# Performance work log

Measured on AMD Instinct MI355X. Metric: run time of the kernel, lower is better.

## Reference

```python
import jax, jax.numpy as jnp
import numpy as np
from jax import lax

EPS = 1e-5
NUM_BITS = 8          # activation quantization bits
NUM_BITS_WEIGHT = 8   # weight quantization bits


def fake_quant(x, bits):
    """Uniform min-max quantize-dequantize (per-tensor), STE on round."""
    mn = jnp.min(x)
    mx = jnp.max(x)
    scale = jnp.maximum((mx - mn) / (2 ** bits - 1), jnp.asarray(1e-8, x.dtype))
    q = jnp.round((x - mn) / scale) * scale + mn
    # straight-through estimator: identity gradient through rounding
    return x + lax.stop_gradient(q - x)


def batchnorm(x, gamma, beta, mean, var):
    # x: [N, C, H, W]; stats per channel C (eval mode, running stats)
    inv = gamma / jnp.sqrt(var + EPS)
    return x * inv[None, :, None, None] + (beta - mean * inv)[None, :, None, None]


def qconv(x, w, padding):
    xq = fake_quant(x, NUM_BITS)
    wq = fake_quant(w, NUM_BITS_WEIGHT)
    return lax.conv_general_dilated(
        xq, wq, window_strides=(1, 1), padding=padding,
        dimension_numbers=("NCHW", "OIHW", "NCHW"))


def setup_inputs() -> dict:
    key = jax.random.key(0)
    ks = jax.random.split(key, 8)
    C_in, bn_size, growth = 512, 4, 32
    C_mid = bn_size * growth  # 128
    N, H, W = 64, 28, 28
    x = jax.random.normal(ks[0], (N, C_in, H, W), dtype=jnp.float32)
    gamma1 = jax.random.uniform(ks[1], (C_in,), minval=0.5, maxval=1.5)
    beta1 = jax.random.normal(ks[2], (C_in,)) * 0.1
    mean1 = jax.random.normal(ks[3], (C_in,)) * 0.1
    var1 = jax.random.uniform(ks[4], (C_in,), minval=0.5, maxval=1.5)
    w1 = jax.random.normal(ks[5], (C_mid, C_in, 1, 1)) * (1.0 / np.sqrt(C_in))
    gamma2 = jax.random.uniform(ks[6], (C_mid,), minval=0.5, maxval=1.5)
    beta2 = jax.random.normal(ks[7], (C_mid,)) * 0.1
    mean2 = jax.random.normal(jax.random.fold_in(key, 10), (C_mid,)) * 0.1
    var2 = jax.random.uniform(jax.random.fold_in(key, 11), (C_mid,), minval=0.5, maxval=1.5)
    w2 = jax.random.normal(jax.random.fold_in(key, 12), (growth, C_mid, 3, 3)) * (1.0 / np.sqrt(C_mid * 9))
    return {"x": x, "gamma1": gamma1, "beta1": beta1, "mean1": mean1, "var1": var1,
            "w1": w1, "gamma2": gamma2, "beta2": beta2, "mean2": mean2, "var2": var2,
            "w2": w2}


def reference(x, gamma1, beta1, mean1, var1, w1, gamma2, beta2, mean2, var2, w2):
    h = jax.nn.relu(batchnorm(x, gamma1, beta1, mean1, var1))
    h = qconv(h, w1, padding=((0, 0), (0, 0)))            # 1x1 conv, 512 -> 128
    h = jax.nn.relu(batchnorm(h, gamma2, beta2, mean2, var2))
    h = qconv(h, w2, padding=((1, 1), (1, 1)))            # 3x3 conv, 128 -> 32
    # drop_rate == 0 -> dropout is identity
    return h
```

## Files before the change

### kernel.cpp

```cpp
#include <hip/hip_runtime.h>

typedef unsigned short u16;
typedef unsigned short u16x4 __attribute__((ext_vector_type(4)));
typedef unsigned short u16x8 __attribute__((ext_vector_type(8)));
typedef short bf16x8 __attribute__((ext_vector_type(8)));
typedef float f32x4 __attribute__((ext_vector_type(4)));

#define EPSF 1e-5f

#define NB   64
#define C1   512
#define C2   128
#define C3   32
#define HH   28
#define WW   28
#define HW   784
#define NHW  50176
#define XELEMS 25690112
#define K1_BLOCKS 2048
#define CONV1_BLOCKS 392
#define CONV2_BLOCKS 784

#define WS_BN1I   64
#define WS_BN1B   2112
#define WS_BN2I   4160
#define WS_BN2B   4672
#define WS_WQ1    5376
#define WS_WQ2    136448
#define WS_P1     210176
#define WS_P2     226560
#define WS_PW1    232832
#define WS_PW2    233344
#define WS_H2     233472

__device__ __forceinline__ float bf2f(u16 u) { return __uint_as_float(((unsigned)u) << 16); }
__device__ __forceinline__ u16 f2bf(float f) {
  unsigned x = __float_as_uint(f);
  return (u16)((x + 0x7fffu + ((x >> 16) & 1u)) >> 16);
}
__device__ __forceinline__ float finz(float f) {
  unsigned u = __float_as_uint(f);
  return ((u & 0x7f800000u) == 0x7f800000u) ? 0.0f : f;
}

__device__ __forceinline__ void block_minmax(float& mn, float& mx) {
  for (int m = 32; m; m >>= 1) {
    mn = fminf(mn, __shfl_xor(mn, m));
    mx = fmaxf(mx, __shfl_xor(mx, m));
  }
  __shared__ float wmn[4], wmx[4];
  const int wv = threadIdx.x >> 6;
  if ((threadIdx.x & 63) == 0) { wmn[wv] = mn; wmx[wv] = mx; }
  __syncthreads();
  if (threadIdx.x == 0) {
    mn = fminf(fminf(wmn[0], wmn[1]), fminf(wmn[2], wmn[3]));
    mx = fmaxf(fmaxf(wmx[0], wmx[1]), fmaxf(wmx[2], wmx[3]));
  }
}

__global__ __launch_bounds__(256) void kwA_kernel(const float* g1, const float* be1,
                                                  const float* m1, const float* v1,
                                                  const float* w1,
                                                  const float* g2, const float* be2,
                                                  const float* m2, const float* v2,
                                                  const float* w2, unsigned char* ws) {
  const int t = threadIdx.x;
  const int b = blockIdx.x;
  float2* pw1 = (float2*)(ws + WS_PW1);
  float2* pw2 = (float2*)(ws + WS_PW2);

  if (b == 80) {
    float* bn1i = (float*)(ws + WS_BN1I);
    float* bn1b = (float*)(ws + WS_BN1B);
    float* bn2i = (float*)(ws + WS_BN2I);
    float* bn2b = (float*)(ws + WS_BN2B);
    for (int c = t; c < C1; c += 256) {
      float inv = g1[c] / sqrtf(v1[c] + EPSF);
      bn1i[c] = inv;
      bn1b[c] = be1[c] - m1[c] * inv;
    }
    if (t < C2) {
      float inv = g2[t] / sqrtf(v2[t] + EPSF);
      bn2i[t] = inv;
      bn2b[t] = be2[t] - m2[t] * inv;
    }
    return;
  }

  float mn = 3.4e38f, mx = -3.4e38f;
  if (b < 64) {
    f32x4 v = *(const f32x4*)(w1 + b * 1024 + t * 4);
#pragma unroll
    for (int j = 0; j < 4; j++) {
      float f = finz(v[j]); mn = fminf(mn, f); mx = fmaxf(mx, f);
    }
    block_minmax(mn, mx);
    if (t == 0) pw1[b] = make_float2(mn, mx);
  } else {
    const int base = (b - 64) * 2304;
#pragma unroll
    for (int j = 0; j < 9; j++) {
      float f = finz(w2[base + t + j * 256]); mn = fminf(mn, f); mx = fmaxf(mx, f);
    }
    block_minmax(mn, mx);
    if (t == 0) pw2[b - 64] = make_float2(mn, mx);
  }
}

__global__ __launch_bounds__(256) void kwB_kernel(const float* w1, const float* w2,
                                                  unsigned char* ws) {
  const float2* pw1 = (const float2*)(ws + WS_PW1);
  const float2* pw2 = (const float2*)(ws + WS_PW2);
  u16* wq1 = (u16*)(ws + WS_WQ1);
  u16* wq2 = (u16*)(ws + WS_WQ2);
  const int t = threadIdx.x;
  const int b = blockIdx.x;
  __shared__ float bc[2];

  if (b < 64) {
    if (t < 64) {
      float2 p = pw1[t];
      float mn = p.x, mx = p.y;
      for (int m = 32; m; m >>= 1) {
        mn = fminf(mn, __shfl_xor(mn, m));
        mx = fmaxf(mx, __shfl_xor(mx, m));
      }
      if (t == 0) { bc[0] = mn; bc[1] = mx; }
    }
    __syncthreads();
    const float mn = bc[0];
    const float s = fmaxf((bc[1] - mn) / 255.0f, 1e-8f);
    const float rs = 1.0f / s;
    f32x4 v = *(const f32x4*)(w1 + b * 1024 + t * 4);
    u16x4 o;
#pragma unroll
    for (int j = 0; j < 4; j++)
      o[j] = f2bf(fmaf(rintf((finz(v[j]) - mn) * rs), s, mn));
    *(u16x4*)(wq1 + b * 1024 + t * 4) = o;
  } else {
    if (t < 64) {
      float2 p = (t < 16) ? pw2[t] : make_float2(3.4e38f, -3.4e38f);
      float mn = p.x, mx = p.y;
      for (int m = 32; m; m >>= 1) {
        mn = fminf(mn, __shfl_xor(mn, m));
        mx = fmaxf(mx, __shfl_xor(mx, m));
      }
      if (t == 0) { bc[0] = mn; bc[1] = mx; }
    }
    __syncthreads();
    const float mn = bc[0];
    const float s = fmaxf((bc[1] - mn) / 255.0f, 1e-8f);
    const float rs = 1.0f / s;
    const int base = (b - 64) * 2304;
#pragma unroll
    for (int j = 0; j < 9; j++) {
      int o = base + t + j * 256;
      int tap = o >> 12;
      int rem = o & 4095;
      float f = finz(w2[rem * 9 + tap]);
      wq2[o] = f2bf(fmaf(rintf((f - mn) * rs), s, mn));
    }
  }
}

__global__ __launch_bounds__(256) void k1_minmax(const float* __restrict__ x, unsigned char* ws) {
  const float* bn1i = (const float*)(ws + WS_BN1I);
  const float* bn1b = (const float*)(ws + WS_BN1B);
  float2* p1 = (float2*)(ws + WS_P1);
  int gid = blockIdx.x * blockDim.x + threadIdx.x;
  int stride = gridDim.x * blockDim.x;
  const int ngroups = XELEMS / 4;
  float mn = 3.4e38f, mx = 0.0f;
  for (int i = gid; i < ngroups; i += stride) {
    int base = i * 4;
    int c = (base / HW) & (C1 - 1);
    float inv = bn1i[c], bb = bn1b[c];
    f32x4 u = *((const f32x4*)x + i);
#pragma unroll
    for (int j = 0; j < 4; j++) {
      float f = fmaxf(fmaf(u[j], inv, bb), 0.0f);
      mn = fminf(mn, f); mx = fmaxf(mx, f);
    }
  }
  block_minmax(mn, mx);
  if (threadIdx.x == 0) p1[blockIdx.x] = make_float2(mn, mx);
}

__global__ __launch_bounds__(256) void conv1_kernel(const float* __restrict__ x,
                                                    unsigned char* ws) {
  const float* bn1i = (const float*)(ws + WS_BN1I);
  const float* bn1b = (const float*)(ws + WS_BN1B);
  const float* bn2i = (const float*)(ws + WS_BN2I);
  const float* bn2b = (const float*)(ws + WS_BN2B);
  const u16* wq1 = (const u16*)(ws + WS_WQ1);
  const float2* p1 = (const float2*)(ws + WS_P1);
  float2* p2 = (float2*)(ws + WS_P2);
  u16* h2 = (u16*)(ws + WS_H2);

  __shared__ __align__(16) u16 Alds[2][128 * 40];
  __shared__ __align__(16) u16 Blds[2][128 * 40];
  __shared__ float bc[2];
  __shared__ float wred[8];

  const int t = threadIdx.x;
  const int sp0 = blockIdx.x * 128;

  {
    float* rmn = (float*)&Alds[0][0];
    float* rmx = (float*)&Blds[0][0];
    const f32x4* p4 = (const f32x4*)p1;
    float mn = 3.4e38f, mx = 0.0f;
#pragma unroll
    for (int i = 0; i < 4; i++) {
      f32x4 v = p4[t + i * 256];
      mn = fminf(mn, fminf(v[0], v[2]));
      mx = fmaxf(mx, fmaxf(v[1], v[3]));
    }
    rmn[t] = mn; rmx[t] = mx;
    __syncthreads();
    for (int s = 128; s > 0; s >>= 1) {
      if (t < s) { rmn[t] = fminf(rmn[t], rmn[t + s]); rmx[t] = fmaxf(rmx[t], rmx[t + s]); }
      __syncthreads();
    }
    if (t == 0) { bc[0] = rmn[0]; bc[1] = rmx[0]; }
    __syncthreads();
  }
  const float mn1 = bc[0];
  const float s1 = fmaxf((bc[1] - mn1) / 255.0f, 1e-8f);
  const float r1 = 1.0f / s1;

  const int kk = t >> 3;
  const int spA = (t & 7) * 8;
  const int spB = 64 + spA;
  const int ga = sp0 + spA, gb = sp0 + spB;
  const int na = ga / HW, hwa = ga % HW;
  const int nb = gb / HW, hwb = gb % HW;
  const float* xA = x + na * (C1 * HW) + hwa;
  const float* xB = x + nb * (C1 * HW) + hwb;
  const int colg = (kk & 7) + 8 * ((((kk >> 3) + (spA >> 3))) & 3);

  const int wco = t >> 1;
  const int wko = (t & 1) * 16;
  const int ab0 = wko >> 3;
  const int aswz = (wco >> 3) & 3;

  const int lane = t & 63;
  const int l15 = lane & 15;
  const int q = lane >> 4;
  const int wv = t >> 6;
  const int wy = wv >> 1;
  const int wx = wv & 1;

  f32x4 acc[4][4] = {};

  u16x8 a0 = *(const u16x8*)(wq1 + wco * C1 + wko);
  u16x8 a1 = *(const u16x8*)(wq1 + wco * C1 + wko + 8);
  f32x4 va0 = *(const f32x4*)(xA + kk * HW);
  f32x4 va1 = *(const f32x4*)(xA + kk * HW + 4);
  f32x4 vb0 = *(const f32x4*)(xB + kk * HW);
  f32x4 vb1 = *(const f32x4*)(xB + kk * HW + 4);
  float inv = bn1i[kk], bb = bn1b[kk];

#pragma unroll 1
  for (int i = 0; i < 16; i++) {
    const int cur = i & 1;
    *(u16x8*)&Alds[cur][wco * 40 + (((ab0 + 0 + aswz) & 3) << 3)] = a0;
    *(u16x8*)&Alds[cur][wco * 40 + (((ab0 + 1 + aswz) & 3) << 3)] = a1;
#pragma unroll
    for (int j = 0; j < 4; j++) {
      float f0 = fmaxf(fmaf(va0[j], inv, bb), 0.0f);
      Blds[cur][(spA + j) * 40 + colg] = f2bf(fmaf(rintf((f0 - mn1) * r1), s1, mn1));
      float f1 = fmaxf(fmaf(va1[j], inv, bb), 0.0f);
      Blds[cur][(spA + 4 + j) * 40 + colg] = f2bf(fmaf(rintf((f1 - mn1) * r1), s1, mn1));
      float g0 = fmaxf(fmaf(vb0[j], inv, bb), 0.0f);
      Blds[cur][(spB + j) * 40 + colg] = f2bf(fmaf(rintf((g0 - mn1) * r1), s1, mn1));
      float g1v = fmaxf(fmaf(vb1[j], inv, bb), 0.0f);
      Blds[cur][(spB + 4 + j) * 40 + colg] = f2bf(fmaf(rintf((g1v - mn1) * r1), s1, mn1));
    }
    if (i < 15) {
      const int kn = (i + 1) * 32;
      a0 = *(const u16x8*)(wq1 + wco * C1 + kn + wko);
      a1 = *(const u16x8*)(wq1 + wco * C1 + kn + wko + 8);
      const int c = kn + kk;
      va0 = *(const f32x4*)(xA + c * HW);
      va1 = *(const f32x4*)(xA + c * HW + 4);
      vb0 = *(const f32x4*)(xB + c * HW);
      vb1 = *(const f32x4*)(xB + c * HW + 4);
      inv = bn1i[c]; bb = bn1b[c];
    }
    __syncthreads();
    bf16x8 af[4], bfr[4];
#pragma unroll
    for (int ii = 0; ii < 4; ii++) {
      int R = wy * 64 + ii * 16 + l15;
      af[ii] = *(const bf16x8*)&Alds[cur][R * 40 + (((q + (R >> 3)) & 3) << 3)];
    }
#pragma unroll
    for (int j = 0; j < 4; j++) {
      int R = wx * 64 + j * 16 + l15;
      bfr[j] = *(const bf16x8*)&Blds[cur][R * 40 + (((q + (R >> 3)) & 3) << 3)];
    }
#pragma unroll
    for (int ii = 0; ii < 4; ii++)
#pragma unroll
      for (int j = 0; j < 4; j++)
        acc[ii][j] = __builtin_amdgcn_mfma_f32_16x16x32_bf16(af[ii], bfr[j], acc[ii][j], 0, 0, 0);
  }

  float lmn = 3.4e38f, lmx = 0.0f;
#pragma unroll
  for (int i = 0; i < 4; i++) {
    int cob = wy * 64 + i * 16 + q * 4;
    f32x4 i2 = *(const f32x4*)&bn2i[cob];
    f32x4 b2 = *(const f32x4*)&bn2b[cob];
#pragma unroll
    for (int j = 0; j < 4; j++) {
      int sp = sp0 + wx * 64 + j * 16 + l15;
      u16x4 v;
#pragma unroll
      for (int r = 0; r < 4; r++) {
        float h = fmaxf(fmaf(acc[i][j][r], i2[r], b2[r]), 0.0f);
        v[r] = f2bf(h);
        lmn = fminf(lmn, h); lmx = fmaxf(lmx, h);
      }
      *(u16x4*)&h2[sp * C2 + cob] = v;
    }
  }
  for (int m = 32; m; m >>= 1) {
    lmn = fminf(lmn, __shfl_xor(lmn, m));
    lmx = fmaxf(lmx, __shfl_xor(lmx, m));
  }
  if (lane == 0) { wred[wv] = lmn; wred[4 + wv] = lmx; }
  __syncthreads();
  if (t == 0) {
    float2 pr;
    pr.x = fminf(fminf(wred[0], wred[1]), fminf(wred[2], wred[3]));
    pr.y = fmaxf(fmaxf(wred[4], wred[5]), fmaxf(wred[6], wred[7]));
    p2[blockIdx.x] = pr;
  }
}

__global__ __launch_bounds__(256) void conv2_kernel(const unsigned char* ws,
                                                    float* __restrict__ out) {
  const u16* wq2 = (const u16*)(ws + WS_WQ2);
  const u16* h2 = (const u16*)(ws + WS_H2);
  const float2* p2 = (const float2*)(ws + WS_P2);
  __shared__ float bc2[2];

  const int t = threadIdx.x;
  {
    float mn = 3.4e38f, mx = 0.0f;
    for (int i = t; i < CONV1_BLOCKS; i += 256) {
      float2 p = p2[i];
      mn = fminf(mn, p.x); mx = fmaxf(mx, p.y);
    }
    block_minmax(mn, mx);
    if (t == 0) { bc2[0] = mn; bc2[1] = mx; }
    __syncthreads();
  }
  const float mn2 = bc2[0];
  const float s2 = fmaxf((bc2[1] - mn2) / 255.0f, 1e-8f);
  const float r2 = 1.0f / s2;

  const int lane = t & 63;
  const int l15 = lane & 15;
  const int q = lane >> 4;
  const int wv = t >> 6;

  const int B = blockIdx.x;
  const int sblk = (B & 7) * 98 + (B >> 3);
  const int spf = sblk * 64 + wv * 16 + l15;
  const int nn = spf / HW;
  const int hwf = spf % HW;
  const int hf = hwf / WW;
  const int wf = hwf % WW;

  f32x4 acc[2] = {};
  bf16x8 bz;
#pragma unroll
  for (int j = 0; j < 8; j++) bz[j] = 0;

  for (int tap = 0; tap < 9; tap++) {
    const int dh = tap / 3 - 1, dw = tap % 3 - 1;
    const u16* wA = wq2 + tap * (C3 * C2);
    unsigned h2i = (unsigned)(hf + dh);
    unsigned w2i = (unsigned)(wf + dw);
    const bool val = (h2i < 28u) && (w2i < 28u);
    const u16* bptr = h2 + ((size_t)(nn * HW + (int)h2i * WW + (int)w2i)) * C2;
#pragma unroll
    for (int ks = 0; ks < C2; ks += 32) {
      bf16x8 a[2], b;
#pragma unroll
      for (int f = 0; f < 2; f++)
        a[f] = *(const bf16x8*)(wA + (f * 16 + l15) * C2 + ks + q * 8);
      if (val) {
        u16x8 hv = *(const u16x8*)(bptr + ks + q * 8);
#pragma unroll
        for (int j = 0; j < 8; j++) {
          float h = bf2f(hv[j]);
          b[j] = (short)f2bf(fmaf(rintf((h - mn2) * r2), s2, mn2));
        }
      } else {
        b = bz;
      }
#pragma unroll
      for (int i = 0; i < 2; i++)
        acc[i] = __builtin_amdgcn_mfma_f32_16x16x32_bf16(a[i], b, acc[i], 0, 0, 0);
    }
  }

#pragma unroll
  for (int i = 0; i < 2; i++) {
    int co = i * 16 + q * 4;
#pragma unroll
    for (int r = 0; r < 4; r++)
      out[(nn * C3 + co + r) * HW + hwf] = acc[i][r];
  }
}

extern "C" void kernel_launch(void* const* d_in, const int* in_sizes, int n_in,
                              void* d_out, int out_size, void* d_ws, size_t ws_size,
                              hipStream_t stream) {
  const float* x  = (const float*)d_in[0];
  const float* g1 = (const float*)d_in[1];
  const float* b1 = (const float*)d_in[2];
  const float* m1 = (const float*)d_in[3];
  const float* v1 = (const float*)d_in[4];
  const float* w1 = (const float*)d_in[5];
  const float* g2 = (const float*)d_in[6];
  const float* b2 = (const float*)d_in[7];
  const float* m2 = (const float*)d_in[8];
  const float* v2 = (const float*)d_in[9];
  const float* w2 = (const float*)d_in[10];
  unsigned char* ws = (unsigned char*)d_ws;
  float* out = (float*)d_out;

  kwA_kernel<<<81, 256, 0, stream>>>(g1, b1, m1, v1, w1, g2, b2, m2, v2, w2, ws);
  kwB_kernel<<<80, 256, 0, stream>>>(w1, w2, ws);
  k1_minmax<<<K1_BLOCKS, 256, 0, stream>>>(x, ws);
  conv1_kernel<<<CONV1_BLOCKS, 256, 0, stream>>>(x, ws);
  conv2_kernel<<<CONV2_BLOCKS, 256, 0, stream>>>(ws, out);
}
```

Measured before the change: 249.2 us.

## Fuse all stages into one persistent kernel with grid barriers

Measured after the change: 591.0 us. 2.37x slower.

```diff
diff --git a/kernel.cpp b/kernel.cpp
--- a/kernel.cpp
+++ b/kernel.cpp
@@ -8,7 +8,6 @@
 
 #define EPSF 1e-5f
 
-#define NB   64
 #define C1   512
 #define C2   128
 #define C3   32
@@ -17,20 +16,20 @@
 #define HW   784
 #define NHW  50176
 #define XELEMS 25690112
-#define K1_BLOCKS 2048
+#define NGROUPS 6422528
+
+#define GRID 512
+#define XBLOCKS 510
+#define W1_BLOCK 510
+#define W2_BLOCK 511
 #define CONV1_BLOCKS 392
-#define CONV2_BLOCKS 784
-
-#define WS_BN1I   64
-#define WS_BN1B   2112
-#define WS_BN2I   4160
-#define WS_BN2B   4672
+#define CONV2_JOBS 784
+
 #define WS_WQ1    5376
 #define WS_WQ2    136448
 #define WS_P1     210176
 #define WS_P2     226560
-#define WS_PW1    232832
-#define WS_PW2    233344
+#define WS_BAR    229696
 #define WS_H2     233472
 
 __device__ __forceinline__ float bf2f(u16 u) { return __uint_as_float(((unsigned)u) << 16); }
@@ -58,363 +57,344 @@
   }
 }
 
-__global__ __launch_bounds__(256) void kwA_kernel(const float* g1, const float* be1,
-                                                  const float* m1, const float* v1,
-                                                  const float* w1,
-                                                  const float* g2, const float* be2,
-                                                  const float* m2, const float* v2,
-                                                  const float* w2, unsigned char* ws) {
+__device__ __forceinline__ void grid_barrier(unsigned* bar, unsigned target) {
+  __syncthreads();
+  if (threadIdx.x == 0) {
+    __threadfence();
+    __hip_atomic_fetch_add(bar, 1u, __ATOMIC_ACQ_REL, __HIP_MEMORY_SCOPE_AGENT);
+    while (__hip_atomic_load(bar, __ATOMIC_ACQUIRE, __HIP_MEMORY_SCOPE_AGENT) < target) {
+      __builtin_amdgcn_s_sleep(2);
+    }
+  }
+  __syncthreads();
+  __threadfence();
+}
+
+__global__ void bar_init_kernel(unsigned char* ws) {
+  if (threadIdx.x == 0) {
+    __hip_atomic_store((unsigned*)(ws + WS_BAR), 0u, __ATOMIC_RELEASE,
+                       __HIP_MEMORY_SCOPE_AGENT);
+  }
+}
+
+__global__ __launch_bounds__(256, 2) void fused_kernel(
+    const float* __restrict__ x, const float* g1, const float* be1,
+    const float* m1, const float* v1, const float* w1,
+    const float* g2, const float* be2, const float* m2, const float* v2,
+    const float* w2, unsigned char* ws, float* __restrict__ out) {
+  __shared__ __align__(16) u16 Alds[2][128 * 40];
+  __shared__ __align__(16) u16 Blds[2][128 * 40];
+  __shared__ float bn1iL[C1], bn1bL[C1];
+  __shared__ float bn2iL[C2], bn2bL[C2];
+  __shared__ float bc[2];
+  __shared__ float wred[8];
+
   const int t = threadIdx.x;
-  const int b = blockIdx.x;
-  float2* pw1 = (float2*)(ws + WS_PW1);
-  float2* pw2 = (float2*)(ws + WS_PW2);
-
-  if (b == 80) {
-    float* bn1i = (float*)(ws + WS_BN1I);
-    float* bn1b = (float*)(ws + WS_BN1B);
-    float* bn2i = (float*)(ws + WS_BN2I);
-    float* bn2b = (float*)(ws + WS_BN2B);
-    for (int c = t; c < C1; c += 256) {
-      float inv = g1[c] / sqrtf(v1[c] + EPSF);
-      bn1i[c] = inv;
-      bn1b[c] = be1[c] - m1[c] * inv;
-    }
-    if (t < C2) {
-      float inv = g2[t] / sqrtf(v2[t] + EPSF);
-      bn2i[t] = inv;
-      bn2b[t] = be2[t] - m2[t] * inv;
-    }
-    return;
-  }
-
-  float mn = 3.4e38f, mx = -3.4e38f;
-  if (b < 64) {
-    f32x4 v = *(const f32x4*)(w1 + b * 1024 + t * 4);
-#pragma unroll
-    for (int j = 0; j < 4; j++) {
-      float f = finz(v[j]); mn = fminf(mn, f); mx = fmaxf(mx, f);
-    }
-    block_minmax(mn, mx);
-    if (t == 0) pw1[b] = make_float2(mn, mx);
-  } else {
-    const int base = (b - 64) * 2304;
-#pragma unroll
-    for (int j = 0; j < 9; j++) {
-      float f = finz(w2[base + t + j * 256]); mn = fminf(mn, f); mx = fmaxf(mx, f);
-    }
-    block_minmax(mn, mx);
-    if (t == 0) pw2[b - 64] = make_float2(mn, mx);
-  }
-}
-
-__global__ __launch_bounds__(256) void kwB_kernel(const float* w1, const float* w2,
-                                                  unsigned char* ws) {
-  const float2* pw1 = (const float2*)(ws + WS_PW1);
-  const float2* pw2 = (const float2*)(ws + WS_PW2);
+  const int bid = blockIdx.x;
+
+  float2* p1 = (float2*)(ws + WS_P1);
+  float2* p2 = (float2*)(ws + WS_P2);
   u16* wq1 = (u16*)(ws + WS_WQ1);
   u16* wq2 = (u16*)(ws + WS_WQ2);
-  const int t = threadIdx.x;
-  const int b = blockIdx.x;
-  __shared__ float bc[2];
-
-  if (b < 64) {
-    if (t < 64) {
-      float2 p = pw1[t];
-      float mn = p.x, mx = p.y;
-      for (int m = 32; m; m >>= 1) {
-        mn = fminf(mn, __shfl_xor(mn, m));
-        mx = fmaxf(mx, __shfl_xor(mx, m));
-      }
+  u16* h2 = (u16*)(ws + WS_H2);
+  unsigned* bar = (unsigned*)(ws + WS_BAR);
+
+  for (int c = t; c < C1; c += 256) {
+    float inv = g1[c] / sqrtf(v1[c] + EPSF);
+    bn1iL[c] = inv;
+    bn1bL[c] = be1[c] - m1[c] * inv;
+  }
+  if (t < C2) {
+    float inv = g2[t] / sqrtf(v2[t] + EPSF);
+    bn2iL[t] = inv;
+    bn2bL[t] = be2[t] - m2[t] * inv;
+  }
+  __syncthreads();
+
+  if (bid < XBLOCKS) {
+    const f32x4* x4 = (const f32x4*)x;
+    float mn = 3.4e38f, mx = 0.0f;
+    auto proc = [&](f32x4 u, int c) {
+      float inv = bn1iL[c], bb = bn1bL[c];
+#pragma unroll
+      for (int j = 0; j < 4; j++) {
+        float f = fmaxf(fmaf(u[j], inv, bb), 0.0f);
+        mn = fminf(mn, f); mx = fmaxf(mx, f);
+      }
+    };
+    const int S = XBLOCKS * 256;
+    int i = bid * 256 + t;
+    for (; i + 3 * S < NGROUPS; i += 4 * S) {
+      f32x4 u0 = x4[i];
+      f32x4 u1 = x4[i + S];
+      f32x4 u2 = x4[i + 2 * S];
+      f32x4 u3 = x4[i + 3 * S];
+      int c0 = (i / 196) & (C1 - 1);
+      int c1 = ((i + S) / 196) & (C1 - 1);
+      int c2 = ((i + 2 * S) / 196) & (C1 - 1);
+      int c3 = ((i + 3 * S) / 196) & (C1 - 1);
+      proc(u0, c0); proc(u1, c1); proc(u2, c2); proc(u3, c3);
+    }
+    for (; i < NGROUPS; i += S) {
+      f32x4 u = x4[i];
+      proc(u, (i / 196) & (C1 - 1));
+    }
+    block_minmax(mn, mx);
+    if (t == 0) p1[bid] = make_float2(mn, mx);
+  } else if (bid == W1_BLOCK) {
+    const f32x4* w4 = (const f32x4*)w1;
+    float mn = 3.4e38f, mx = -3.4e38f;
+#pragma unroll 8
+    for (int k = t; k < 16384; k += 256) {
+      f32x4 v = w4[k];
+#pragma unroll
+      for (int j = 0; j < 4; j++) {
+        float f = finz(v[j]); mn = fminf(mn, f); mx = fmaxf(mx, f);
+      }
+    }
+    block_minmax(mn, mx);
+    if (t == 0) { bc[0] = mn; bc[1] = mx; }
+    __syncthreads();
+    const float mnv = bc[0];
+    const float s = fmaxf((bc[1] - mnv) / 255.0f, 1e-8f);
+    const float rs = 1.0f / s;
+#pragma unroll 4
+    for (int k = t; k < 16384; k += 256) {
+      f32x4 v = w4[k];
+      u16x4 o;
+#pragma unroll
+      for (int j = 0; j < 4; j++)
+        o[j] = f2bf(fmaf(rintf((finz(v[j]) - mnv) * rs), s, mnv));
+      *(u16x4*)(wq1 + k * 4) = o;
+    }
+  } else {
+    const f32x4* w4 = (const f32x4*)w2;
+    float mn = 3.4e38f, mx = -3.4e38f;
+#pragma unroll 4
+    for (int k = t; k < 9216; k += 256) {
+      f32x4 v = w4[k];
+#pragma unroll
+      for (int j = 0; j < 4; j++) {
+        float f = finz(v[j]); mn = fminf(mn, f); mx = fmaxf(mx, f);
+      }
+    }
+    block_minmax(mn, mx);
+    if (t == 0) { bc[0] = mn; bc[1] = mx; }
+    __syncthreads();
+    const float mnv = bc[0];
+    const float s = fmaxf((bc[1] - mnv) / 255.0f, 1e-8f);
+    const float rs = 1.0f / s;
+    for (int jj = t; jj < 36864; jj += 256) {
+      int tap = jj >> 12;
+      int rem = jj & 4095;
+      float f = finz(w2[rem * 9 + tap]);
+      wq2[jj] = f2bf(fmaf(rintf((f - mnv) * rs), s, mnv));
+    }
+  }
+
+  grid_barrier(bar, GRID);
+
+  if (bid < CONV1_BLOCKS) {
+    const int sp0 = bid * 128;
+
+    {
+      float mn = 3.4e38f, mx = 0.0f;
+      for (int i = t; i < XBLOCKS; i += 256) {
+        float2 p = p1[i];
+        mn = fminf(mn, p.x); mx = fmaxf(mx, p.y);
+      }
+      block_minmax(mn, mx);
       if (t == 0) { bc[0] = mn; bc[1] = mx; }
-    }
+      __syncthreads();
+    }
+    const float mn1 = bc[0];
+    const float s1 = fmaxf((bc[1] - mn1) / 255.0f, 1e-8f);
+    const float r1 = 1.0f / s1;
+
+    const int kk = t >> 3;
+    const int spA = (t & 7) * 8;
+    const int spB = 64 + spA;
+    const int ga = sp0 + spA, gb = sp0 + spB;
+    const int na = ga / HW, hwa = ga % HW;
+    const int nb = gb / HW, hwb = gb % HW;
+    const float* xA = x + na * (C1 * HW) + hwa;
+    const float* xB = x + nb * (C1 * HW) + hwb;
+    const int colg = (kk & 7) + 8 * ((((kk >> 3) + (spA >> 3))) & 3);
+
+    const int wco = t >> 1;
+    const int wko = (t & 1) * 16;
+    const int ab0 = wko >> 3;
+    const int aswz = (wco >> 3) & 3;
+
+    const int lane = t & 63;
+    const int l15 = lane & 15;
+    const int q = lane >> 4;
+    const int wv = t >> 6;
+    const int wy = wv >> 1;
+    const int wx = wv & 1;
+
+    f32x4 acc[4][4] = {};
+
+    u16x8 a0 = *(const u16x8*)(wq1 + wco * C1 + wko);
+    u16x8 a1 = *(const u16x8*)(wq1 + wco * C1 + wko + 8);
+    f32x4 va0 = *(const f32x4*)(xA + kk * HW);
+    f32x4 va1 = *(const f32x4*)(xA + kk * HW + 4);
+    f32x4 vb0 = *(const f32x4*)(xB + kk * HW);
+    f32x4 vb1 = *(const f32x4*)(xB + kk * HW + 4);
+    float inv = bn1iL[kk], bb = bn1bL[kk];
+
+#pragma unroll 1
+    for (int i = 0; i < 16; i++) {
+      const int cur = i & 1;
+      *(u16x8*)&Alds[cur][wco * 40 + (((ab0 + 0 + aswz) & 3) << 3)] = a0;
+      *(u16x8*)&Alds[cur][wco * 40 + (((ab0 + 1 + aswz) & 3) << 3)] = a1;
+#pragma unroll
+      for (int j = 0; j < 4; j++) {
+        float f0 = fmaxf(fmaf(va0[j], inv, bb), 0.0f);
+        Blds[cur][(spA + j) * 40 + colg] = f2bf(fmaf(rintf((f0 - mn1) * r1), s1, mn1));
+        float f1 = fmaxf(fmaf(va1[j], inv, bb), 0.0f);
+        Blds[cur][(spA + 4 + j) * 40 + colg] = f2bf(fmaf(rintf((f1 - mn1) * r1), s1, mn1));
+        float g0 = fmaxf(fmaf(vb0[j], inv, bb), 0.0f);
+        Blds[cur][(spB + j) * 40 + colg] = f2bf(fmaf(rintf((g0 - mn1) * r1), s1, mn1));
+        float g1v = fmaxf(fmaf(vb1[j], inv, bb), 0.0f);
+        Blds[cur][(spB + 4 + j) * 40 + colg] = f2bf(fmaf(rintf((g1v - mn1) * r1), s1, mn1));
+      }
+      if (i < 15) {
+        const int kn = (i + 1) * 32;
+        a0 = *(const u16x8*)(wq1 + wco * C1 + kn + wko);
+        a1 = *(const u16x8*)(wq1 + wco * C1 + kn + wko + 8);
+        const int c = kn + kk;
+        va0 = *(const f32x4*)(xA + c * HW);
+        va1 = *(const f32x4*)(xA + c * HW + 4);
+        vb0 = *(const f32x4*)(xB + c * HW);
+        vb1 = *(const f32x4*)(xB + c * HW + 4);
+        inv = bn1iL[c]; bb = bn1bL[c];
+      }
+      __syncthreads();
+      bf16x8 af[4], bfr[4];
+#pragma unroll
+      for (int ii = 0; ii < 4; ii++) {
+        int R = wy * 64 + ii * 16 + l15;
+        af[ii] = *(const bf16x8*)&Alds[cur][R * 40 + (((q + (R >> 3)) & 3) << 3)];
+      }
+#pragma unroll
+      for (int j = 0; j < 4; j++) {
+        int R = wx * 64 + j * 16 + l15;
+        bfr[j] = *(const bf16x8*)&Blds[cur][R * 40 + (((q + (R >> 3)) & 3) << 3)];
+      }
+#pragma unroll
+      for (int ii = 0; ii < 4; ii++)
+#pragma unroll
+        for (int j = 0; j < 4; j++)
+          acc[ii][j] = __builtin_amdgcn_mfma_f32_16x16x32_bf16(af[ii], bfr[j], acc[ii][j], 0, 0, 0);
+    }
+
+    float lmn = 3.4e38f, lmx = 0.0f;
+#pragma unroll
+    for (int i = 0; i < 4; i++) {
+      int cob = wy * 64 + i * 16 + q * 4;
+      f32x4 i2 = *(const f32x4*)&bn2iL[cob];
+      f32x4 b2 = *(const f32x4*)&bn2bL[cob];
+#pragma unroll
+      for (int j = 0; j < 4; j++) {
+        int sp = sp0 + wx * 64 + j * 16 + l15;
+        u16x4 v;
+#pragma unroll
+        for (int r = 0; r < 4; r++) {
+          float h = fmaxf(fmaf(acc[i][j][r], i2[r], b2[r]), 0.0f);
+          v[r] = f2bf(h);
+          lmn = fminf(lmn, h); lmx = fmaxf(lmx, h);
+        }
+        *(u16x4*)&h2[sp * C2 + cob] = v;
+      }
+    }
+    for (int m = 32; m; m >>= 1) {
+      lmn = fminf(lmn, __shfl_xor(lmn, m));
+      lmx = fmaxf(lmx, __shfl_xor(lmx, m));
+    }
+    if (lane == 0) { wred[wv] = lmn; wred[4 + wv] = lmx; }
     __syncthreads();
-    const float mn = bc[0];
-    const float s = fmaxf((bc[1] - mn) / 255.0f, 1e-8f);
-    const float rs = 1.0f / s;
-    f32x4 v = *(const f32x4*)(w1 + b * 1024 + t * 4);
-    u16x4 o;
-#pragma unroll
-    for (int j = 0; j < 4; j++)
-      o[j] = f2bf(fmaf(rintf((finz(v[j]) - mn) * rs), s, mn));
-    *(u16x4*)(wq1 + b * 1024 + t * 4) = o;
-  } else {
-    if (t < 64) {
-      float2 p = (t < 16) ? pw2[t] : make_float2(3.4e38f, -3.4e38f);
-      float mn = p.x, mx = p.y;
-      for (int m = 32; m; m >>= 1) {
-        mn = fminf(mn, __shfl_xor(mn, m));
-        mx = fmaxf(mx, __shfl_xor(mx, m));
-      }
+    if (t == 0) {
+      float2 pr;
+      pr.x = fminf(fminf(wred[0], wred[1]), fminf(wred[2], wred[3]));
+      pr.y = fmaxf(fmaxf(wred[4], wred[5]), fmaxf(wred[6], wred[7]));
+      p2[bid] = pr;
+    }
+  }
+
+  grid_barrier(bar, 2 * GRID);
+
+  {
+    {
+      float mn = 3.4e38f, mx = 0.0f;
+      for (int i = t; i < CONV1_BLOCKS; i += 256) {
+        float2 p = p2[i];
+        mn = fminf(mn, p.x); mx = fmaxf(mx, p.y);
+      }
+      block_minmax(mn, mx);
       if (t == 0) { bc[0] = mn; bc[1] = mx; }
-    }
-    __syncthreads();
-    const float mn = bc[0];
-    const float s = fmaxf((bc[1] - mn) / 255.0f, 1e-8f);
-    const float rs = 1.0f / s;
-    const int base = (b - 64) * 2304;
-#pragma unroll
-    for (int j = 0; j < 9; j++) {
-      int o = base + t + j * 256;
-      int tap = o >> 12;
-      int rem = o & 4095;
-      float f = finz(w2[rem * 9 + tap]);
-      wq2[o] = f2bf(fmaf(rintf((f - mn) * rs), s, mn));
-    }
-  }
-}
-
-__global__ __launch_bounds__(256) void k1_minmax(const float* __restrict__ x, unsigned char* ws) {
-  const float* bn1i = (const float*)(ws + WS_BN1I);
-  const float* bn1b = (const float*)(ws + WS_BN1B);
-  float2* p1 = (float2*)(ws + WS_P1);
-  int gid = blockIdx.x * blockDim.x + threadIdx.x;
-  int stride = gridDim.x * blockDim.x;
-  const int ngroups = XELEMS / 4;
-  float mn = 3.4e38f, mx = 0.0f;
-  for (int i = gid; i < ngroups; i += stride) {
-    int base = i * 4;
-    int c = (base / HW) & (C1 - 1);
-    float inv = bn1i[c], bb = bn1b[c];
-    f32x4 u = *((const f32x4*)x + i);
-#pragma unroll
-    for (int j = 0; j < 4; j++) {
-      float f = fmaxf(fmaf(u[j], inv, bb), 0.0f);
-      mn = fminf(mn, f); mx = fmaxf(mx, f);
-    }
-  }
-  block_minmax(mn, mx);
-  if (threadIdx.x == 0) p1[blockIdx.x] = make_float2(mn, mx);
-}
-
-__global__ __launch_bounds__(256) void conv1_kernel(const float* __restrict__ x,
-                                                    unsigned char* ws) {
-  const float* bn1i = (const float*)(ws + WS_BN1I);
-  const float* bn1b = (const float*)(ws + WS_BN1B);
-  const float* bn2i = (const float*)(ws + WS_BN2I);
-  const float* bn2b = (const float*)(ws + WS_BN2B);
-  const u16* wq1 = (const u16*)(ws + WS_WQ1);
-  const float2* p1 = (const float2*)(ws + WS_P1);
-  float2* p2 = (float2*)(ws + WS_P2);
-  u16* h2 = (u16*)(ws + WS_H2);
-
-  __shared__ __align__(16) u16 Alds[2][128 * 40];
-  __shared__ __align__(16) u16 Blds[2][128 * 40];
-  __shared__ float bc[2];
-  __shared__ float wred[8];
-
-  const int t = threadIdx.x;
-  const int sp0 = blockIdx.x * 128;
-
-  {
-    float* rmn = (float*)&Alds[0][0];
-    float* rmx = (float*)&Blds[0][0];
-    const f32x4* p4 = (const f32x4*)p1;
-    float mn = 3.4e38f, mx = 0.0f;
-#pragma unroll
-    for (int i = 0; i < 4; i++) {
-      f32x4 v = p4[t + i * 256];
-      mn = fminf(mn, fminf(v[0], v[2]));
-      mx = fmaxf(mx, fmaxf(v[1], v[3]));
-    }
-    rmn[t] = mn; rmx[t] = mx;
-    __syncthreads();
-    for (int s = 128; s > 0; s >>= 1) {
-      if (t < s) { rmn[t] = fminf(rmn[t], rmn[t + s]); rmx[t] = fmaxf(rmx[t], rmx[t + s]); }
       __syncthreads();
     }
-    if (t == 0) { bc[0] = rmn[0]; bc[1] = rmx[0]; }
-    __syncthreads();
-  }
-  const float mn1 = bc[0];
-  const float s1 = fmaxf((bc[1] - mn1) / 255.0f, 1e-8f);
-  const float r1 = 1.0f / s1;
-
-  const int kk = t >> 3;
-  const int spA = (t & 7) * 8;
-  const int spB = 64 + spA;
-  const int ga = sp0 + spA, gb = sp0 + spB;
-  const int na = ga / HW, hwa = ga % HW;
-  const int nb = gb / HW, hwb = gb % HW;
-  const float* xA = x + na * (C1 * HW) + hwa;
-  const float* xB = x + nb * (C1 * HW) + hwb;
-  const int colg = (kk & 7) + 8 * ((((kk >> 3) + (spA >> 3))) & 3);
-
-  const int wco = t >> 1;
-  const int wko = (t & 1) * 16;
-  const int ab0 = wko >> 3;
-  const int aswz = (wco >> 3) & 3;
-
-  const int lane = t & 63;
-  const int l15 = lane & 15;
-  const int q = lane >> 4;
-  const int wv = t >> 6;
-  const int wy = wv >> 1;
-  const int wx = wv & 1;
-
-  f32x4 acc[4][4] = {};
-
-  u16x8 a0 = *(const u16x8*)(wq1 + wco * C1 + wko);
-  u16x8 a1 = *(const u16x8*)(wq1 + wco * C1 + wko + 8);
-  f32x4 va0 = *(const f32x4*)(xA + kk * HW);
-  f32x4 va1 = *(const f32x4*)(xA + kk * HW + 4);
-  f32x4 vb0 = *(const f32x4*)(xB + kk * HW);
-  f32x4 vb1 = *(const f32x4*)(xB + kk * HW + 4);
-  float inv = bn1i[kk], bb = bn1b[kk];
-
-#pragma unroll 1
-  for (int i = 0; i < 16; i++) {
-    const int cur = i & 1;
-    *(u16x8*)&Alds[cur][wco * 40 + (((ab0 + 0 + aswz) & 3) << 3)] = a0;
-    *(u16x8*)&Alds[cur][wco * 40 + (((ab0 + 1 + aswz) & 3) << 3)] = a1;
-#pragma unroll
-    for (int j = 0; j < 4; j++) {
-      float f0 = fmaxf(fmaf(va0[j], inv, bb), 0.0f);
-      Blds[cur][(spA + j) * 40 + colg] = f2bf(fmaf(rintf((f0 - mn1) * r1), s1, mn1));
-      float f1 = fmaxf(fmaf(va1[j], inv, bb), 0.0f);
-      Blds[cur][(spA + 4 + j) * 40 + colg] = f2bf(fmaf(rintf((f1 - mn1) * r1), s1, mn1));
-      float g0 = fmaxf(fmaf(vb0[j], inv, bb), 0.0f);
-      Blds[cur][(spB + j) * 40 + colg] = f2bf(fmaf(rintf((g0 - mn1) * r1), s1, mn1));
-      float g1v = fmaxf(fmaf(vb1[j], inv, bb), 0.0f);
-      Blds[cur][(spB + 4 + j) * 40 + colg] = f2bf(fmaf(rintf((g1v - mn1) * r1), s1, mn1));
-    }
-    if (i < 15) {
-      const int kn = (i + 1) * 32;
-      a0 = *(const u16x8*)(wq1 + wco * C1 + kn + wko);
-      a1 = *(const u16x8*)(wq1 + wco * C1 + kn + wko + 8);
-      const int c = kn + kk;
-      va0 = *(const f32x4*)(xA + c * HW);
-      va1 = *(const f32x4*)(xA + c * HW + 4);
-      vb0 = *(const f32x4*)(xB + c * HW);
-      vb1 = *(const f32x4*)(xB + c * HW + 4);
-      inv = bn1i[c]; bb = bn1b[c];
-    }
-    __syncthreads();
-    bf16x8 af[4], bfr[4];
-#pragma unroll
-    for (int ii = 0; ii < 4; ii++) {
-      int R = wy * 64 + ii * 16 + l15;
-      af[ii] = *(const bf16x8*)&Alds[cur][R * 40 + (((q + (R >> 3)) & 3) << 3)];
-    }
-#pragma unroll
-    for (int j = 0; j < 4; j++) {
-      int R = wx * 64 + j * 16 + l15;
-      bfr[j] = *(const bf16x8*)&Blds[cur][R * 40 + (((q + (R >> 3)) & 3) << 3)];
-    }
-#pragma unroll
-    for (int ii = 0; ii < 4; ii++)
-#pragma unroll
-      for (int j = 0; j < 4; j++)
-        acc[ii][j] = __builtin_amdgcn_mfma_f32_16x16x32_bf16(af[ii], bfr[j], acc[ii][j], 0, 0, 0);
-  }
-
-  float lmn = 3.4e38f, lmx = 0.0f;
-#pragma unroll
-  for (int i = 0; i < 4; i++) {
-    int cob = wy * 64 + i * 16 + q * 4;
-    f32x4 i2 = *(const f32x4*)&bn2i[cob];
-    f32x4 b2 = *(const f32x4*)&bn2b[cob];
-#pragma unroll
-    for (int j = 0; j < 4; j++) {
-      int sp = sp0 + wx * 64 + j * 16 + l15;
-      u16x4 v;
-#pragma unroll
-      for (int r = 0; r < 4; r++) {
-        float h = fmaxf(fmaf(acc[i][j][r], i2[r], b2[r]), 0.0f);
-        v[r] = f2bf(h);
-        lmn = fminf(lmn, h); lmx = fmaxf(lmx, h);
-      }
-      *(u16x4*)&h2[sp * C2 + cob] = v;
-    }
-  }
-  for (int m = 32; m; m >>= 1) {
-    lmn = fminf(lmn, __shfl_xor(lmn, m));
-    lmx = fmaxf(lmx, __shfl_xor(lmx, m));
-  }
-  if (lane == 0) { wred[wv] = lmn; wred[4 + wv] = lmx; }
-  __syncthreads();
-  if (t == 0) {
-    float2 pr;
-    pr.x = fminf(fminf(wred[0], wred[1]), fminf(wred[2], wred[3]));
-    pr.y = fmaxf(fmaxf(wred[4], wred[5]), fmaxf(wred[6], wred[7]));
-    p2[blockIdx.x] = pr;
-  }
-}
-
-__global__ __launch_bounds__(256) void conv2_kernel(const unsigned char* ws,
-                                                    float* __restrict__ out) {
-  const u16* wq2 = (const u16*)(ws + WS_WQ2);
-  const u16* h2 = (const u16*)(ws + WS_H2);
-  const float2* p2 = (const float2*)(ws + WS_P2);
-  __shared__ float bc2[2];
-
-  const int t = threadIdx.x;
-  {
-    float mn = 3.4e38f, mx = 0.0f;
-    for (int i = t; i < CONV1_BLOCKS; i += 256) {
-      float2 p = p2[i];
-      mn = fminf(mn, p.x); mx = fmaxf(mx, p.y);
-    }
-    block_minmax(mn, mx);
-    if (t == 0) { bc2[0] = mn; bc2[1] = mx; }
-    __syncthreads();
-  }
-  const float mn2 = bc2[0];
-  const float s2 = fmaxf((bc2[1] - mn2) / 255.0f, 1e-8f);
-  const float r2 = 1.0f / s2;
-
-  const int lane = t & 63;
-  const int l15 = lane & 15;
-  const int q = lane >> 4;
-  const int wv = t >> 6;
-
-  const int B = blockIdx.x;
-  const int sblk = (B & 7) * 98 + (B >> 3);
-  const int spf = sblk * 64 + wv * 16 + l15;
-  const int nn = spf / HW;
-  const int hwf = spf % HW;
-  const int hf = hwf / WW;
-  const int wf = hwf % WW;
-
-  f32x4 acc[2] = {};
-  bf16x8 bz;
-#pragma unroll
-  for (int j = 0; j < 8; j++) bz[j] = 0;
-
-  for (int tap = 0; tap < 9; tap++) {
-    const int dh = tap / 3 - 1, dw = tap % 3 - 1;
-    const u16* wA = wq2 + tap * (C3 * C2);
-    unsigned h2i = (unsigned)(hf + dh);
-    unsigned w2i = (unsigned)(wf + dw);
-    const bool val = (h2i < 28u) && (w2i < 28u);
-    const u16* bptr = h2 + ((size_t)(nn * HW + (int)h2i * WW + (int)w2i)) * C2;
-#pragma unroll
-    for (int ks = 0; ks < C2; ks += 32) {
-      bf16x8 a[2], b;
-#pragma unroll
-      for (int f = 0; f < 2; f++)
-        a[f] = *(const bf16x8*)(wA + (f * 16 + l15) * C2 + ks + q * 8);
-      if (val) {
-        u16x8 hv = *(const u16x8*)(bptr + ks + q * 8);
-#pragma unroll
-        for (int j = 0; j < 8; j++) {
-          float h = bf2f(hv[j]);
-          b[j] = (short)f2bf(fmaf(rintf((h - mn2) * r2), s2, mn2));
+    const float mn2 = bc[0];
+    const float s2 = fmaxf((bc[1] - mn2) / 255.0f, 1e-8f);
+    const float r2 = 1.0f / s2;
+
+    const int lane = t & 63;
+    const int l15 = lane & 15;
+    const int q = lane >> 4;
+    const int wv = t >> 6;
+
+    bf16x8 bz;
+#pragma unroll
+    for (int j = 0; j < 8; j++) bz[j] = 0;
+
+    for (int job = bid; job < CONV2_JOBS; job += GRID) {
+      const int sblk = (job & 7) * 98 + (job >> 3);
+      const int spf = sblk * 64 + wv * 16 + l15;
+      const int nn = spf / HW;
+      const int hwf = spf % HW;
+      const int hf = hwf / WW;
+      const int wf = hwf % WW;
+
+      f32x4 acc[2] = {};
+
+      for (int tap = 0; tap < 9; tap++) {
+        const int dh = tap / 3 - 1, dw = tap % 3 - 1;
+        const u16* wA = wq2 + tap * (C3 * C2);
+        unsigned h2i = (unsigned)(hf + dh);
+        unsigned w2i = (unsigned)(wf + dw);
+        const bool val = (h2i < 28u) && (w2i < 28u);
+        const u16* bptr = h2 + ((size_t)(nn * HW + (int)h2i * WW + (int)w2i)) * C2;
+#pragma unroll
+        for (int ks = 0; ks < C2; ks += 32) {
+          bf16x8 a[2], b;
+#pragma unroll
+          for (int f = 0; f < 2; f++)
+            a[f] = *(const bf16x8*)(wA + (f * 16 + l15) * C2 + ks + q * 8);
+          if (val) {
+            u16x8 hv = *(const u16x8*)(bptr + ks + q * 8);
+#pragma unroll
+            for (int j = 0; j < 8; j++) {
+              float h = bf2f(hv[j]);
+              b[j] = (short)f2bf(fmaf(rintf((h - mn2) * r2), s2, mn2));
+            }
+          } else {
+            b = bz;
+          }
+#pragma unroll
+          for (int i = 0; i < 2; i++)
+            acc[i] = __builtin_amdgcn_mfma_f32_16x16x32_bf16(a[i], b, acc[i], 0, 0, 0);
         }
-      } else {
-        b = bz;
-      }
-#pragma unroll
-      for (int i = 0; i < 2; i++)
-        acc[i] = __builtin_amdgcn_mfma_f32_16x16x32_bf16(a[i], b, acc[i], 0, 0, 0);
-    }
-  }
-
-#pragma unroll
-  for (int i = 0; i < 2; i++) {
-    int co = i * 16 + q * 4;
-#pragma unroll
-    for (int r = 0; r < 4; r++)
-      out[(nn * C3 + co + r) * HW + hwf] = acc[i][r];
+      }
+
+#pragma unroll
+      for (int i = 0; i < 2; i++) {
+        int co = i * 16 + q * 4;
+#pragma unroll
+        for (int r = 0; r < 4; r++)
+          out[(nn * C3 + co + r) * HW + hwf] = acc[i][r];
+      }
+    }
   }
 }
 
@@ -435,9 +415,7 @@
   unsigned char* ws = (unsigned char*)d_ws;
   float* out = (float*)d_out;
 
-  kwA_kernel<<<81, 256, 0, stream>>>(g1, b1, m1, v1, w1, g2, b2, m2, v2, w2, ws);
-  kwB_kernel<<<80, 256, 0, stream>>>(w1, w2, ws);
-  k1_minmax<<<K1_BLOCKS, 256, 0, stream>>>(x, ws);
-  conv1_kernel<<<CONV1_BLOCKS, 256, 0, stream>>>(x, ws);
-  conv2_kernel<<<CONV2_BLOCKS, 256, 0, stream>>>(ws, out);
-}
+  bar_init_kernel<<<1, 64, 0, stream>>>(ws);
+  fused_kernel<<<GRID, 256, 0, stream>>>(x, g1, b1, m1, v1, w1, g2, b2, m2, v2,
+                                         w2, ws, out);
+}
```
